# Kernel tuning notes

Measured on AMD Instinct MI355X. Metric: run time of the kernel, lower is better.

The kernel has to match this reference:

```python
import jax, jax.numpy as jnp
import numpy as np

B, T, D = 2, 2048, 1024
HEADS = 16
MEM = 512
HEAD_DIM = D // HEADS


def setup_inputs() -> dict:
    key = jax.random.key(0)
    k1, k2, k3, k4, k5 = jax.random.split(key, 5)
    x = jax.random.normal(k1, (B, T, D), dtype=jnp.float32)
    w_qkv = jax.random.normal(k2, (3 * D, D), dtype=jnp.float32) * (1.0 / np.sqrt(D))
    w_out = jax.random.normal(k3, (D, D), dtype=jnp.float32) * (1.0 / np.sqrt(D))
    b_out = jax.random.normal(k4, (D,), dtype=jnp.float32) * 0.01
    memory = jax.random.normal(k5, (MEM, D), dtype=jnp.float32)
    return {"x": x, "w_qkv": w_qkv, "w_out": w_out, "b_out": b_out, "memory": memory}


def reference(x, w_qkv, w_out, b_out, memory):
    b, t, d = x.shape
    h, hd = HEADS, HEAD_DIM
    scale = hd ** -0.5
    # QKV projection: [B,T,3D]
    qkv = jnp.einsum('btd,ed->bte', x, w_qkv)
    q, k, v = jnp.split(qkv, 3, axis=-1)
    # [B,H,T,hd]
    q = q.reshape(b, t, h, hd).transpose(0, 2, 1, 3)
    k = k.reshape(b, t, h, hd).transpose(0, 2, 1, 3)
    v = v.reshape(b, t, h, hd).transpose(0, 2, 1, 3)
    # memory K/V: [B,H,MEM,hd] (broadcast over batch)
    mem = memory.reshape(1, MEM, h, hd).transpose(0, 2, 1, 3)
    mem = jnp.broadcast_to(mem, (b, h, MEM, hd))
    k = jnp.concatenate([mem, k], axis=2)
    v = jnp.concatenate([mem, v], axis=2)
    # attention: scores [B,H,T,MEM+T]
    scores = jnp.einsum('bhqd,bhkd->bhqk', q, k) * scale
    weights = jax.nn.softmax(scores, axis=-1)
    out = jnp.einsum('bhqk,bhkd->bhqd', weights, v)
    out = out.transpose(0, 2, 1, 3).reshape(b, t, d)
    return jnp.einsum('btd,ed->bte', out, w_out) + b_out
```

## Files before the change

kernel.cpp:

```cpp
#include <hip/hip_runtime.h>
#include <hip/hip_bf16.h>
#include <stdint.h>

#define B_   2
#define T_   2048
#define D_   1024
#define H_   16
#define HD_  64
#define MEM_ 512
#define KV_  (MEM_ + T_)
#define NIT_ (KV_ / 64)

using bf16 = __bf16;
typedef __bf16 bf16x8 __attribute__((ext_vector_type(8)));
typedef float  f32x4  __attribute__((ext_vector_type(4)));
typedef short  s16x4  __attribute__((ext_vector_type(4)));
typedef short  s16x8  __attribute__((ext_vector_type(8)));

__device__ __forceinline__ f32x4 mfma16(bf16x8 a, bf16x8 b, f32x4 c) {
  return __builtin_amdgcn_mfma_f32_16x16x32_bf16(a, b, c, 0, 0, 0);
}

__device__ __forceinline__ void gll16(const void* g, void* l) {
  __builtin_amdgcn_global_load_lds(
      (const __attribute__((address_space(1))) unsigned int*)g,
      (__attribute__((address_space(3))) unsigned int*)l, 16, 0, 0);
}

__device__ __forceinline__ unsigned short bf16_bits(float f) {
  bf16 h = (bf16)f;
  return __builtin_bit_cast(unsigned short, h);
}

__device__ __forceinline__ ushort4 pack4(f32x4 v) {
  ushort4 p;
  p.x = bf16_bits(v[0]); p.y = bf16_bits(v[1]);
  p.z = bf16_bits(v[2]); p.w = bf16_bits(v[3]);
  return p;
}

__device__ __forceinline__ bf16x8 cvt8(f32x4 a, f32x4 b) {
  bf16x8 r;
  r[0] = (bf16)a[0]; r[1] = (bf16)a[1]; r[2] = (bf16)a[2]; r[3] = (bf16)a[3];
  r[4] = (bf16)b[0]; r[5] = (bf16)b[1]; r[6] = (bf16)b[2]; r[7] = (bf16)b[3];
  return r;
}

__global__ void prep(const float* __restrict__ x, const float* __restrict__ wq,
                     const float* __restrict__ memory,
                     const float* __restrict__ wout,
                     bf16* __restrict__ xb, bf16* __restrict__ wqb,
                     bf16* __restrict__ mem_k, bf16* __restrict__ mem_vt,
                     bf16* __restrict__ wob) {
  int blk = blockIdx.x;
  if (blk < 3584) {
    const float* s = (blk < 2048) ? x : wq;
    bf16* d = (blk < 2048) ? xb : wqb;
    size_t i = ((size_t)(blk < 2048 ? blk : blk - 2048) * 256 + threadIdx.x) * 8;
    f32x4 a = *(const f32x4*)(s + i);
    f32x4 b = *(const f32x4*)(s + i + 4);
    *(bf16x8*)(d + i) = cvt8(a, b);
  } else if (blk < 3840) {
    int idx8 = ((blk - 3584) * 256 + threadIdx.x) * 8;
    int m = idx8 >> 10, d0 = idx8 & 1023;
    int hh = d0 >> 6, hd0 = d0 & 63;
    f32x4 a = *(const f32x4*)(memory + idx8);
    f32x4 b = *(const f32x4*)(memory + idx8 + 4);
    *(bf16x8*)&mem_k[((size_t)hh * MEM_ + m) * HD_ + hd0] = cvt8(a, b);
  } else if (blk < 4096) {
    int idx = (blk - 3840) * 256 + threadIdx.x;
    int d = idx & 1023;
    int m0 = (idx >> 10) * 8;
    bf16x8 r;
#pragma unroll
    for (int j = 0; j < 8; j++)
      r[j] = (bf16)memory[(size_t)(m0 + j) * D_ + d];
    *(bf16x8*)&mem_vt[(size_t)d * MEM_ + m0] = r;
  } else {
    size_t i = ((size_t)(blk - 4096) * 256 + threadIdx.x) * 8;
    f32x4 a = *(const f32x4*)(wout + i);
    f32x4 b = *(const f32x4*)(wout + i + 4);
    *(bf16x8*)(wob + i) = cvt8(a, b);
  }
}

__global__ void conv_bf16(const float* __restrict__ s, bf16* __restrict__ d) {
  size_t i = ((size_t)blockIdx.x * 256 + threadIdx.x) * 8;
  f32x4 a = *(const f32x4*)(s + i);
  f32x4 b = *(const f32x4*)(s + i + 4);
  *(bf16x8*)(d + i) = cvt8(a, b);
}

template <int EPI, bool APLANE, int NTILE>
__global__ __launch_bounds__(256, 3) void gemm_bt(
    const bf16* __restrict__ A, const bf16* __restrict__ W,
    const float* __restrict__ bias,
    bf16* __restrict__ q_ws, bf16* __restrict__ k_ws, bf16* __restrict__ vt_ws,
    float* __restrict__ Cout, int K) {
  constexpr int NF = NTILE / 32;
  constexpr int NB = NTILE / 32;
  __shared__ __align__(16) bf16 Als[128 * 64];
  __shared__ __align__(16) bf16 Bls[NTILE * 64];
  char* AB = (char*)Als;
  char* BB = (char*)Bls;
  const int nwg = gridDim.x * gridDim.y;
  int lin = blockIdx.y * gridDim.x + blockIdx.x;
  lin = (lin & 7) * (nwg >> 3) + (lin >> 3);
  const int m0 = (lin / gridDim.x) * 128;
  const int n0 = (lin % gridDim.x) * NTILE;
  const int tid = threadIdx.x;
  const int w = tid >> 6;
  const int lane = tid & 63;
  const int lx = lane & 15;
  const int quad = lane >> 4;
  const int amb = (w & 1) * 64;
  const int bnb = (w >> 1) * (NTILE / 2);
  const int srow = tid >> 3;
  const int cs = (tid & 7) ^ (srow & 7);

  f32x4 acc[4][NF];
#pragma unroll
  for (int i = 0; i < 4; i++)
#pragma unroll
    for (int j = 0; j < NF; j++) acc[i][j] = (f32x4){0.f, 0.f, 0.f, 0.f};

  for (int k0 = 0; k0 < K; k0 += 64) {
    const bf16* pa[4];
#pragma unroll
    for (int g = 0; g < 4; g++) {
      int r = srow + 32 * g;
      if constexpr (APLANE) {
        int hh = k0 >> 6, hd = cs * 8;
        int mA = m0 + r;
        pa[g] = A + ((size_t)((mA >> 11) * H_ + hh) * T_ + (mA & 2047)) * HD_ + hd;
      } else {
        pa[g] = A + (size_t)(m0 + r) * K + k0 + cs * 8;
      }
    }
    const bf16* pb[NB];
#pragma unroll
    for (int g = 0; g < NB; g++)
      pb[g] = W + (size_t)(n0 + srow + 32 * g) * K + k0 + cs * 8;

    __syncthreads();
#pragma unroll
    for (int g = 0; g < 4; g++) gll16(pa[g], AB + g * 4096 + tid * 16);
#pragma unroll
    for (int g = 0; g < NB; g++) gll16(pb[g], BB + g * 4096 + tid * 16);
    __syncthreads();

    bf16x8 af[4][2], bfr[NF][2];
    const int rk = (lx & 7) << 4;
#pragma unroll
    for (int mt = 0; mt < 4; mt++)
#pragma unroll
      for (int kh = 0; kh < 2; kh++)
        af[mt][kh] = *(const bf16x8*)(AB + (size_t)(amb + mt * 16 + lx) * 128 +
                                      ((quad * 16 + kh * 64) ^ rk));
#pragma unroll
    for (int nt = 0; nt < NF; nt++)
#pragma unroll
      for (int kh = 0; kh < 2; kh++)
        bfr[nt][kh] = *(const bf16x8*)(BB + (size_t)(bnb + nt * 16 + lx) * 128 +
                                       ((quad * 16 + kh * 64) ^ rk));
#pragma unroll
    for (int kh = 0; kh < 2; kh++)
#pragma unroll
      for (int mt = 0; mt < 4; mt++)
#pragma unroll
        for (int nt = 0; nt < NF; nt++)
          acc[mt][nt] = mfma16(af[mt][kh], bfr[nt][kh], acc[mt][nt]);
  }

  if (EPI == 0) {
#pragma unroll
    for (int mt = 0; mt < 4; mt++) {
      int mbase = m0 + amb + mt * 16 + quad * 4;
      int b = mbase >> 11;
      int t = mbase & 2047;
#pragma unroll
      for (int nt = 0; nt < NF; nt++) {
        int col = n0 + bnb + nt * 16 + lx;
        int which = col >> 10;
        int d = col & 1023;
        int hh = d >> 6, hdi = d & 63;
        int bh = b * H_ + hh;
        if (which == 0) {
#pragma unroll
          for (int r = 0; r < 4; r++)
            q_ws[((size_t)bh * T_ + t + r) * HD_ + hdi] = (bf16)acc[mt][nt][r];
        } else if (which == 1) {
#pragma unroll
          for (int r = 0; r < 4; r++)
            k_ws[((size_t)bh * T_ + t + r) * HD_ + hdi] = (bf16)acc[mt][nt][r];
        } else {
          *(ushort4*)&vt_ws[((size_t)bh * HD_ + hdi) * T_ + t] =
              pack4(acc[mt][nt]);
        }
      }
    }
  } else {
#pragma unroll
    for (int nt = 0; nt < NF; nt++) {
      int col = n0 + bnb + nt * 16 + lx;
      float bias_f = bias[col];
#pragma unroll
      for (int mt = 0; mt < 4; mt++) {
        int mbase = m0 + amb + mt * 16 + quad * 4;
#pragma unroll
        for (int r = 0; r < 4; r++)
          Cout[(size_t)(mbase + r) * D_ + col] = acc[mt][nt][r] + bias_f;
      }
    }
  }
}

__global__ __launch_bounds__(256, 2) void attn_kernel(
    bf16* __restrict__ q_ws, const bf16* __restrict__ k_ws,
    const bf16* __restrict__ vt_ws, const bf16* __restrict__ mem_k,
    const bf16* __restrict__ mem_vt) {
  __shared__ __align__(16) bf16 Kls[2 * 64 * 64];
  __shared__ __align__(16) bf16 Vls[2 * 64 * 64];
  char* KB = (char*)Kls;
  char* VB = (char*)Vls;
  const int tid = threadIdx.x;
  const int w = tid >> 6;
  const int lane = tid & 63;
  const int lx = lane & 15;
  const int quad = lane >> 4;
  const int bh = blockIdx.x & 31;
  const int qt = blockIdx.x >> 5;
  const int q0 = qt * 128 + w * 32;
  const int h = bh & 15;

  const int srow1 = tid >> 3;
  const int sc1 = (tid & 7) ^ (srow1 & 7);

  bf16* qbase = q_ws + ((size_t)bh * T_ + q0) * HD_;

  const bf16* kpl = k_ws + (size_t)bh * T_ * HD_;
  const bf16* vpl = vt_ws + (size_t)bh * HD_ * T_;
  const bf16* mkp = mem_k + (size_t)h * MEM_ * HD_;
  const bf16* mvp = mem_vt + (size_t)h * HD_ * MEM_;

  auto stage = [&](int it2, int bi) {
    const int kv0 = it2 * 64;
    const bf16 *kp1, *kp2, *vp1, *vp2;
    if (kv0 < MEM_) {
      kp1 = mkp + (size_t)(kv0 + srow1) * HD_ + sc1 * 8;
      kp2 = kp1 + (size_t)32 * HD_;
      vp1 = mvp + (size_t)srow1 * MEM_ + kv0 + sc1 * 8;
      vp2 = vp1 + (size_t)32 * MEM_;
    } else {
      const int t0 = kv0 - MEM_;
      kp1 = kpl + (size_t)(t0 + srow1) * HD_ + sc1 * 8;
      kp2 = kp1 + (size_t)32 * HD_;
      vp1 = vpl + (size_t)srow1 * T_ + t0 + sc1 * 8;
      vp2 = vp1 + (size_t)32 * T_;
    }
    char* kb = KB + bi * 8192;
    char* vb = VB + bi * 8192;
    gll16(kp1, kb + tid * 16);
    gll16(kp2, kb + tid * 16 + 4096);
    gll16(vp1, vb + tid * 16);
    gll16(vp2, vb + tid * 16 + 4096);
  };

  const float QSCALE = 0.125f * 1.44269504089f;
  bf16x8 qf[2][2];
#pragma unroll
  for (int qg = 0; qg < 2; qg++)
#pragma unroll
    for (int hf = 0; hf < 2; hf++) {
      bf16x8 v = *(const bf16x8*)(qbase + (size_t)(qg * 16 + lx) * HD_ +
                                  hf * 32 + quad * 8);
#pragma unroll
      for (int i = 0; i < 8; i++)
        v[i] = (bf16)((float)v[i] * QSCALE);
      qf[qg][hf] = v;
    }

  bf16x8 ones;
#pragma unroll
  for (int i = 0; i < 8; i++) ones[i] = (bf16)1.0f;

  f32x4 o[4][2];
#pragma unroll
  for (int mt = 0; mt < 4; mt++)
#pragma unroll
    for (int qg = 0; qg < 2; qg++) o[mt][qg] = (f32x4){0.f, 0.f, 0.f, 0.f};
  f32x4 osum[2] = {(f32x4){0.f, 0.f, 0.f, 0.f}, (f32x4){0.f, 0.f, 0.f, 0.f}};

  stage(0, 0);

  for (int it = 0; it < NIT_; it++) {
    const int cur = it & 1;
    if (it + 1 < NIT_) {
      stage(it + 1, cur ^ 1);
      asm volatile("s_waitcnt vmcnt(4)" ::: "memory");
    } else {
      asm volatile("s_waitcnt vmcnt(0)" ::: "memory");
    }
    __builtin_amdgcn_s_barrier();
    __builtin_amdgcn_sched_barrier(0);

    const char* KBc = KB + cur * 8192;
    const char* VBc = VB + cur * 8192;
    const int sw = (lx & 7) << 4;
    f32x4 s[4][2];
    __builtin_amdgcn_s_setprio(1);
#pragma unroll
    for (int g = 0; g < 4; g++) {
      const char* kb = KBc + (size_t)(g * 16 + lx) * 128;
      bf16x8 ka0 = *(const bf16x8*)(kb + ((quad * 16) ^ sw));
      bf16x8 ka1 = *(const bf16x8*)(kb + ((64 + quad * 16) ^ sw));
#pragma unroll
      for (int qg = 0; qg < 2; qg++) {
        s[g][qg] = (f32x4){0.f, 0.f, 0.f, 0.f};
        s[g][qg] = mfma16(ka0, qf[qg][0], s[g][qg]);
        s[g][qg] = mfma16(ka1, qf[qg][1], s[g][qg]);
      }
    }
    __builtin_amdgcn_s_setprio(0);

    s16x8 pk[2][2];
#pragma unroll
    for (int qg = 0; qg < 2; qg++) {
#pragma unroll
      for (int g = 0; g < 4; g++) {
#pragma unroll
        for (int r = 0; r < 4; r++) {
          float p = __builtin_amdgcn_exp2f(s[g][qg][r]);
          pk[qg][g >> 1][(g & 1) * 4 + r] = (short)bf16_bits(p);
        }
      }
    }

    __builtin_amdgcn_s_setprio(1);
#pragma unroll
    for (int mt = 0; mt < 4; mt++) {
      const char* vb = VBc + (size_t)(mt * 16 + lx) * 128;
#pragma unroll
      for (int p = 0; p < 2; p++) {
        s16x4 lo = *(const s16x4*)(vb + ((p * 64 + quad * 8) ^ sw));
        s16x4 hi = *(const s16x4*)(vb + ((p * 64 + 32 + quad * 8) ^ sw));
        s16x8 cat = __builtin_shufflevector(lo, hi, 0, 1, 2, 3, 4, 5, 6, 7);
        bf16x8 va = __builtin_bit_cast(bf16x8, cat);
#pragma unroll
        for (int qg = 0; qg < 2; qg++)
          o[mt][qg] = mfma16(va, __builtin_bit_cast(bf16x8, pk[qg][p]),
                             o[mt][qg]);
      }
    }
#pragma unroll
    for (int p = 0; p < 2; p++)
#pragma unroll
      for (int qg = 0; qg < 2; qg++)
        osum[qg] = mfma16(ones, __builtin_bit_cast(bf16x8, pk[qg][p]),
                          osum[qg]);
    __builtin_amdgcn_s_setprio(0);

    __builtin_amdgcn_sched_barrier(0);
    __builtin_amdgcn_s_barrier();
  }

  float inv[2] = {1.f / osum[0][0], 1.f / osum[1][0]};

#pragma unroll
  for (int qg = 0; qg < 2; qg++) {
#pragma unroll
    for (int mt = 0; mt < 4; mt++) {
      f32x4 ov;
#pragma unroll
      for (int r = 0; r < 4; r++) ov[r] = o[mt][qg][r] * inv[qg];
      *(ushort4*)(qbase + (size_t)(qg * 16 + lx) * HD_ + mt * 16 + quad * 4)
          = pack4(ov);
    }
  }
}

extern "C" void kernel_launch(void* const* d_in, const int* in_sizes, int n_in,
                              void* d_out, int out_size, void* d_ws,
                              size_t ws_size, hipStream_t stream) {
  const float* x      = (const float*)d_in[0];
  const float* w_qkv  = (const float*)d_in[1];
  const float* w_out  = (const float*)d_in[2];
  const float* b_out  = (const float*)d_in[3];
  const float* memory = (const float*)d_in[4];

  char* ws = (char*)d_ws;
  bf16* q_ws   = (bf16*)(ws);
  bf16* k_ws   = (bf16*)(ws + (8u << 20));
  bf16* vt_ws  = (bf16*)(ws + (16u << 20));
  bf16* mem_k  = (bf16*)(ws + (24u << 20));
  bf16* mem_vt = (bf16*)(ws + (25u << 20));
  float* out = (float*)d_out;

  char* outc = (char*)d_out;
  bf16* xb  = (bf16*)(outc);
  bf16* wqb = (bf16*)(outc + (8u << 20));

  const bool big_ws = ws_size >= (28u << 20);
  bf16* wob = big_ws ? (bf16*)(ws + (26u << 20))
                     : (bf16*)(ws + (8u << 20));

  prep<<<dim3(big_ws ? 4608 : 4096), dim3(256), 0, stream>>>(
      x, w_qkv, memory, w_out, xb, wqb, mem_k, mem_vt, wob);
  gemm_bt<0, false, 128><<<dim3(24, 32), dim3(256), 0, stream>>>(
      xb, wqb, nullptr, q_ws, k_ws, vt_ws, nullptr, 1024);
  attn_kernel<<<dim3(512), dim3(256), 0, stream>>>(
      q_ws, k_ws, vt_ws, mem_k, mem_vt);
  if (!big_ws)
    conv_bf16<<<dim3(512), dim3(256), 0, stream>>>(w_out, wob);
  gemm_bt<1, true, 64><<<dim3(16, 32), dim3(256), 0, stream>>>(
      q_ws, wob, b_out, nullptr, nullptr, nullptr, out, 1024);
}
```

Measured before the change: 184.6 us.

## Split attention KV range across two warp-groups per block and merge via LDS

Result: faster. 179.5 us (-2.8%).

```diff
diff --git a/kernel.cpp b/kernel.cpp
--- a/kernel.cpp
+++ b/kernel.cpp
@@ -10,6 +10,7 @@
 #define MEM_ 512
 #define KV_  (MEM_ + T_)
 #define NIT_ (KV_ / 64)
+#define NIT2_ (NIT_ / 2)
 
 using bf16 = __bf16;
 typedef __bf16 bf16x8 __attribute__((ext_vector_type(8)));
@@ -215,16 +216,18 @@
   }
 }
 
-__global__ __launch_bounds__(256, 2) void attn_kernel(
+__global__ __launch_bounds__(512, 4) void attn_kernel(
     bf16* __restrict__ q_ws, const bf16* __restrict__ k_ws,
     const bf16* __restrict__ vt_ws, const bf16* __restrict__ mem_k,
     const bf16* __restrict__ mem_vt) {
-  __shared__ __align__(16) bf16 Kls[2 * 64 * 64];
-  __shared__ __align__(16) bf16 Vls[2 * 64 * 64];
+  __shared__ __align__(16) bf16 Kls[2 * 2 * 64 * 64];
+  __shared__ __align__(16) bf16 Vls[2 * 2 * 64 * 64];
   char* KB = (char*)Kls;
   char* VB = (char*)Vls;
   const int tid = threadIdx.x;
-  const int w = tid >> 6;
+  const int wh = tid >> 8;
+  const int t2 = tid & 255;
+  const int w = t2 >> 6;
   const int lane = tid & 63;
   const int lx = lane & 15;
   const int quad = lane >> 4;
@@ -233,8 +236,11 @@
   const int q0 = qt * 128 + w * 32;
   const int h = bh & 15;
 
-  const int srow1 = tid >> 3;
-  const int sc1 = (tid & 7) ^ (srow1 & 7);
+  const int srow1 = t2 >> 3;
+  const int sc1 = (t2 & 7) ^ (srow1 & 7);
+
+  char* KBh = KB + wh * 16384;
+  char* VBh = VB + wh * 16384;
 
   bf16* qbase = q_ws + ((size_t)bh * T_ + q0) * HD_;
 
@@ -244,7 +250,7 @@
   const bf16* mvp = mem_vt + (size_t)h * HD_ * MEM_;
 
   auto stage = [&](int it2, int bi) {
-    const int kv0 = it2 * 64;
+    const int kv0 = (wh * NIT2_ + it2) * 64;
     const bf16 *kp1, *kp2, *vp1, *vp2;
     if (kv0 < MEM_) {
       kp1 = mkp + (size_t)(kv0 + srow1) * HD_ + sc1 * 8;
@@ -258,12 +264,12 @@
       vp1 = vpl + (size_t)srow1 * T_ + t0 + sc1 * 8;
       vp2 = vp1 + (size_t)32 * T_;
     }
-    char* kb = KB + bi * 8192;
-    char* vb = VB + bi * 8192;
-    gll16(kp1, kb + tid * 16);
-    gll16(kp2, kb + tid * 16 + 4096);
-    gll16(vp1, vb + tid * 16);
-    gll16(vp2, vb + tid * 16 + 4096);
+    char* kb = KBh + bi * 8192;
+    char* vb = VBh + bi * 8192;
+    gll16(kp1, kb + t2 * 16);
+    gll16(kp2, kb + t2 * 16 + 4096);
+    gll16(vp1, vb + t2 * 16);
+    gll16(vp2, vb + t2 * 16 + 4096);
   };
 
   const float QSCALE = 0.125f * 1.44269504089f;
@@ -293,9 +299,9 @@
 
   stage(0, 0);
 
-  for (int it = 0; it < NIT_; it++) {
+  for (int it = 0; it < NIT2_; it++) {
     const int cur = it & 1;
-    if (it + 1 < NIT_) {
+    if (it + 1 < NIT2_) {
       stage(it + 1, cur ^ 1);
       asm volatile("s_waitcnt vmcnt(4)" ::: "memory");
     } else {
@@ -304,8 +310,8 @@
     __builtin_amdgcn_s_barrier();
     __builtin_amdgcn_sched_barrier(0);
 
-    const char* KBc = KB + cur * 8192;
-    const char* VBc = VB + cur * 8192;
+    const char* KBc = KBh + cur * 8192;
+    const char* VBc = VBh + cur * 8192;
     const int sw = (lx & 7) << 4;
     f32x4 s[4][2];
     __builtin_amdgcn_s_setprio(1);
@@ -364,17 +370,37 @@
     __builtin_amdgcn_s_barrier();
   }
 
-  float inv[2] = {1.f / osum[0][0], 1.f / osum[1][0]};
-
-#pragma unroll
-  for (int qg = 0; qg < 2; qg++) {
-#pragma unroll
-    for (int mt = 0; mt < 4; mt++) {
-      f32x4 ov;
-#pragma unroll
-      for (int r = 0; r < 4; r++) ov[r] = o[mt][qg][r] * inv[qg];
-      *(ushort4*)(qbase + (size_t)(qg * 16 + lx) * HD_ + mt * 16 + quad * 4)
-          = pack4(ov);
+  float* OS = (float*)KB;
+  float* OSS = (float*)VB;
+  if (wh == 1) {
+    float* dst = OS + t2 * 32;
+#pragma unroll
+    for (int mt = 0; mt < 4; mt++)
+#pragma unroll
+      for (int qg = 0; qg < 2; qg++) {
+        int c = mt * 2 + qg;
+        *(f32x4*)(dst + ((c ^ (t2 & 7)) * 4)) = o[mt][qg];
+      }
+    OSS[t2 * 2 + 0] = osum[0][0];
+    OSS[t2 * 2 + 1] = osum[1][0];
+  }
+  __syncthreads();
+  if (wh == 0) {
+    const float* src = OS + t2 * 32;
+    float inv[2] = {1.f / (osum[0][0] + OSS[t2 * 2 + 0]),
+                    1.f / (osum[1][0] + OSS[t2 * 2 + 1])};
+#pragma unroll
+    for (int qg = 0; qg < 2; qg++) {
+#pragma unroll
+      for (int mt = 0; mt < 4; mt++) {
+        int c = mt * 2 + qg;
+        f32x4 po = *(const f32x4*)(src + ((c ^ (t2 & 7)) * 4));
+        f32x4 ov;
+#pragma unroll
+        for (int r = 0; r < 4; r++) ov[r] = (o[mt][qg][r] + po[r]) * inv[qg];
+        *(ushort4*)(qbase + (size_t)(qg * 16 + lx) * HD_ + mt * 16 + quad * 4)
+            = pack4(ov);
+      }
     }
   }
 }
@@ -408,7 +434,7 @@
       x, w_qkv, memory, w_out, xb, wqb, mem_k, mem_vt, wob);
   gemm_bt<0, false, 128><<<dim3(24, 32), dim3(256), 0, stream>>>(
       xb, wqb, nullptr, q_ws, k_ws, vt_ws, nullptr, 1024);
-  attn_kernel<<<dim3(512), dim3(256), 0, stream>>>(
+  attn_kernel<<<dim3(512), dim3(512), 0, stream>>>(
       q_ws, k_ws, vt_ws, mem_k, mem_vt);
   if (!big_ws)
     conv_bf16<<<dim3(512), dim3(256), 0, stream>>>(w_out, wob);
```
